# Kernel optimization log

Measured on AMD Instinct MI355X. Metric: run time of the kernel, lower is better.

## Reference

```python
import jax, jax.numpy as jnp
import numpy as np


def setup_inputs() -> dict:
    key = jax.random.key(0)
    k1, k2 = jax.random.split(key)
    B, C, H, W = 4, 64, 256, 256
    x = jax.random.normal(k1, (B, C, H, W), dtype=jnp.float32)
    perspective = jax.random.uniform(k2, (B, 1, H, W), dtype=jnp.float32)
    alpha = jnp.ones((1,), dtype=jnp.float32) * 3.0   # sigma scale
    beta = jnp.ones((1,), dtype=jnp.float32)          # sigmoid slope
    gamma = jnp.zeros((1,), dtype=jnp.float32)        # sigmoid shift
    return {"x": x, "perspective": perspective, "alpha": alpha,
            "beta": beta, "gamma": gamma, "kernel_size": 7}


def reference(x, perspective, alpha, beta, gamma, kernel_size):
    K = int(kernel_size)
    pad = K // 2
    B, C, H, W = x.shape
    # AdaptiveSigmoid sigma map, clamped like the torch module
    sigma = jnp.maximum(alpha * jax.nn.sigmoid(beta * perspective + gamma), 1e-4)  # [B,1,H,W]
    inv2s2 = 1.0 / (2.0 * sigma * sigma)                                           # [B,1,H,W]
    # squared distance of each kernel tap from center (static)
    offs = np.arange(K) - pad
    d2 = (offs[:, None] ** 2 + offs[None, :] ** 2).reshape(-1).astype(np.float32)  # [K*K]
    # per-pixel, per-tap Gaussian weights, normalized over taps
    w = jnp.exp(-d2[:, None, None, None, None] * inv2s2[None])  # [K*K,B,1,H,W]
    w = w / jnp.sum(w, axis=0)
    xp = jnp.pad(x, ((0, 0), (0, 0), (pad, pad), (pad, pad)))
    out = jnp.zeros_like(x)
    k = 0
    for i in range(K):            # fixed small K*K loop (49 taps), jit-friendly
        for j in range(K):
            out = out + w[k] * xp[:, :, i:i + H, j:j + W]
            k += 1
    return out
```

## Files before the change

kernel.cpp:

```cpp
#include <hip/hip_runtime.h>

#define NB 4
#define NC 64
#define NH 256
#define NW 256
#define TH 32
#define SROWS (TH + 6)
#define LROW 264

__global__ __launch_bounds__(256)
void wprep(const float* __restrict__ persp,
           const float* __restrict__ alpha_p,
           const float* __restrict__ beta_p,
           const float* __restrict__ gamma_p,
           float* __restrict__ ws)
{
    const float alpha = alpha_p[0];
    const float beta  = beta_p[0];
    const float gamma = gamma_p[0];
    const int i = (blockIdx.x * 256 + threadIdx.x) * 4;
    const float4 p = *(const float4*)(persp + i);
    const float pa[4] = {p.x, p.y, p.z, p.w};
    float g[4], inv2[4];
    #pragma unroll
    for (int k = 0; k < 4; ++k) {
        const float z  = fmaf(beta, pa[k], gamma);
        const float sg = __builtin_amdgcn_rcpf(1.0f + __expf(-z));
        const float sigma = fmaxf(alpha * sg, 1e-4f);
        const float t  = 0.5f * __builtin_amdgcn_rcpf(sigma * sigma);
        const float gg = __expf(-t);
        const float g2 = gg * gg;
        const float p4 = g2 * g2;
        const float p9 = p4 * p4 * gg;
        const float S  = fmaf(2.0f, (gg + p4) + p9, 1.0f);
        const float inv = __builtin_amdgcn_rcpf(S);
        g[k] = gg;
        inv2[k] = inv * inv;
    }
    float* wp = ws + (size_t)i * 2;
    *(float4*)(wp)     = make_float4(g[0], inv2[0], g[1], inv2[1]);
    *(float4*)(wp + 4) = make_float4(g[2], inv2[2], g[3], inv2[3]);
}

__global__ __launch_bounds__(256, 2)
void adaptive_gauss7(const float* __restrict__ x,
                     const float* __restrict__ wsr,
                     float* __restrict__ out)
{
    __shared__ float lds[SROWS * LROW];

    const int tid  = threadIdx.x;
    const int lane = tid & 63;
    const int wv   = tid >> 6;
    const int c    = blockIdx.x;
    const int h0   = blockIdx.y * TH;
    const int b    = blockIdx.z;
    const int colbase = lane * 4;
    const int rg      = h0 + wv * 8;

    const float* xc   = x   + (size_t)(b * NC + c) * NH * NW;
    float*       outp = out + (size_t)(b * NC + c) * NH * NW;
    const float* wrow = wsr + (size_t)b * NH * NW * 2;

    if (tid < SROWS) {
        *(float4*)&lds[tid * LROW]       = make_float4(0.f, 0.f, 0.f, 0.f);
        *(float4*)&lds[tid * LROW + 260] = make_float4(0.f, 0.f, 0.f, 0.f);
    }

    for (int r = wv; r < SROWS; r += 4) {
        const int gr = h0 - 3 + r;
        if ((unsigned)gr < NH) {
            __builtin_amdgcn_global_load_lds(
                (const __attribute__((address_space(1))) void*)(xc + (size_t)gr * NW + colbase),
                (__attribute__((address_space(3))) void*)&lds[r * LROW + 4],
                16, 0, 0);
        } else {
            *(float4*)&lds[r * LROW + 4 + colbase] = make_float4(0.f, 0.f, 0.f, 0.f);
        }
    }
    __syncthreads();

    float win[7][12];
    #pragma unroll
    for (int r = 0; r < 7; ++r) {
        const float* rp = &lds[(wv * 8 + r) * LROW + colbase];
        const float4 a0 = *(const float4*)(rp);
        const float4 a1 = *(const float4*)(rp + 4);
        const float4 a2 = *(const float4*)(rp + 8);
        win[r][0] = a0.x; win[r][1] = a0.y; win[r][2]  = a0.z; win[r][3]  = a0.w;
        win[r][4] = a1.x; win[r][5] = a1.y; win[r][6]  = a1.z; win[r][7]  = a1.w;
        win[r][8] = a2.x; win[r][9] = a2.y; win[r][10] = a2.z; win[r][11] = a2.w;
    }

    const float* wp0 = wrow + ((size_t)rg * NW + colbase) * 2;
    float4 wa = *(const float4*)(wp0);
    float4 wb = *(const float4*)(wp0 + 4);

    #pragma unroll
    for (int o = 0; o < 8; ++o) {
        float nxt[12];
        if (o < 7) {
            const float* rp = &lds[(wv * 8 + o + 7) * LROW + colbase];
            const float4 a0 = *(const float4*)(rp);
            const float4 a1 = *(const float4*)(rp + 4);
            const float4 a2 = *(const float4*)(rp + 8);
            nxt[0] = a0.x; nxt[1] = a0.y; nxt[2]  = a0.z; nxt[3]  = a0.w;
            nxt[4] = a1.x; nxt[5] = a1.y; nxt[6]  = a1.z; nxt[7]  = a1.w;
            nxt[8] = a2.x; nxt[9] = a2.y; nxt[10] = a2.z; nxt[11] = a2.w;
        }
        float4 na, nb;
        if (o < 7) {
            const float* wp = wrow + ((size_t)(rg + o + 1) * NW + colbase) * 2;
            na = *(const float4*)(wp);
            nb = *(const float4*)(wp + 4);
        }

        const float gk[4] = {wa.x, wa.z, wb.x, wb.z};
        const float iv[4] = {wa.y, wa.w, wb.y, wb.w};
        float res[4];
        #pragma unroll
        for (int k = 0; k < 4; ++k) {
            const float g  = gk[k];
            const float g2 = g * g;
            const float p4 = g2 * g2;
            const float p9 = p4 * p4 * g;

            float rs[7];
            #pragma unroll
            for (int j = 0; j < 7; ++j) {
                const int s = (o + j) % 7;
                rs[j] = fmaf(p9, win[s][k+1] + win[s][k+7],
                        fmaf(p4, win[s][k+2] + win[s][k+6],
                        fmaf(g,  win[s][k+3] + win[s][k+5],
                                 win[s][k+4])));
            }
            const float acc = fmaf(p9, rs[0] + rs[6],
                              fmaf(p4, rs[1] + rs[5],
                              fmaf(g,  rs[2] + rs[4],
                                       rs[3])));
            res[k] = acc * iv[k];
        }
        *(float4*)(outp + (size_t)(rg + o) * NW + colbase) =
            make_float4(res[0], res[1], res[2], res[3]);

        if (o < 7) {
            #pragma unroll
            for (int q = 0; q < 12; ++q)
                win[o % 7][q] = nxt[q];
            wa = na; wb = nb;
        }
    }
}

extern "C" void kernel_launch(void* const* d_in, const int* in_sizes, int n_in,
                              void* d_out, int out_size, void* d_ws, size_t ws_size,
                              hipStream_t stream) {
    const float* x     = (const float*)d_in[0];
    const float* persp = (const float*)d_in[1];
    const float* alpha = (const float*)d_in[2];
    const float* beta  = (const float*)d_in[3];
    const float* gamma = (const float*)d_in[4];
    float* outp        = (float*)d_out;
    float* ws          = (float*)d_ws;

    wprep<<<dim3((NB * NH * NW) / 1024), dim3(256), 0, stream>>>(persp, alpha, beta, gamma, ws);
    adaptive_gauss7<<<dim3(NC, NH / TH, NB), dim3(256), 0, stream>>>(x, ws, outp);
}
```

Measured before the change: 137.6 us.

## Halve row tile and compute output rows in pairs streaming LDS rows once

The row tile shrinks from 32 to 16, so each wave produces 4 output rows instead of 8 and the grid gets twice as many blocks. Instead of keeping a rotating 7-row register window, each pair of output rows streams 8 LDS rows once and accumulates symmetric vertical partial sums on the fly. Weight loads for all four rows are issued before the LDS fill to hide global latency. The aim is lower register pressure and more parallelism, at the cost of a larger halo-overhead fraction (22/16 rows loaded vs 38/32) and more LDS reads per output.

```diff
diff --git a/kernel.cpp b/kernel.cpp
--- a/kernel.cpp
+++ b/kernel.cpp
@@ -4,7 +4,7 @@
 #define NC 64
 #define NH 256
 #define NW 256
-#define TH 32
+#define TH 16
 #define SROWS (TH + 6)
 #define LROW 264
 
@@ -56,11 +56,19 @@
     const int h0   = blockIdx.y * TH;
     const int b    = blockIdx.z;
     const int colbase = lane * 4;
-    const int rg      = h0 + wv * 8;
+    const int rg      = h0 + wv * 4;
 
     const float* xc   = x   + (size_t)(b * NC + c) * NH * NW;
     float*       outp = out + (size_t)(b * NC + c) * NH * NW;
     const float* wrow = wsr + (size_t)b * NH * NW * 2;
+
+    float4 wsv[8];
+    #pragma unroll
+    for (int o = 0; o < 4; ++o) {
+        const float* wp = wrow + ((size_t)(rg + o) * NW + colbase) * 2;
+        wsv[2 * o]     = *(const float4*)(wp);
+        wsv[2 * o + 1] = *(const float4*)(wp + 4);
+    }
 
     if (tid < SROWS) {
         *(float4*)&lds[tid * LROW]       = make_float4(0.f, 0.f, 0.f, 0.f);
@@ -80,75 +88,86 @@
     }
     __syncthreads();
 
-    float win[7][12];
     #pragma unroll
-    for (int r = 0; r < 7; ++r) {
-        const float* rp = &lds[(wv * 8 + r) * LROW + colbase];
-        const float4 a0 = *(const float4*)(rp);
-        const float4 a1 = *(const float4*)(rp + 4);
-        const float4 a2 = *(const float4*)(rp + 8);
-        win[r][0] = a0.x; win[r][1] = a0.y; win[r][2]  = a0.z; win[r][3]  = a0.w;
-        win[r][4] = a1.x; win[r][5] = a1.y; win[r][6]  = a1.z; win[r][7]  = a1.w;
-        win[r][8] = a2.x; win[r][9] = a2.y; win[r][10] = a2.z; win[r][11] = a2.w;
-    }
+    for (int half = 0; half < 2; ++half) {
+        const int o0 = 2 * half;
+        const float4 wa0 = wsv[2 * o0],     wb0 = wsv[2 * o0 + 1];
+        const float4 wa1 = wsv[2 * o0 + 2], wb1 = wsv[2 * o0 + 3];
+        const float g0_[4] = {wa0.x, wa0.z, wb0.x, wb0.z};
+        const float i0_[4] = {wa0.y, wa0.w, wb0.y, wb0.w};
+        const float g1_[4] = {wa1.x, wa1.z, wb1.x, wb1.z};
+        const float i1_[4] = {wa1.y, wa1.w, wb1.y, wb1.w};
+        float g0[4], p40[4], p90[4], g1[4], p41[4], p91[4];
+        #pragma unroll
+        for (int k = 0; k < 4; ++k) {
+            g0[k] = g0_[k];
+            const float t = g0[k] * g0[k];
+            p40[k] = t * t;
+            p90[k] = p40[k] * p40[k] * g0[k];
+            g1[k] = g1_[k];
+            const float u = g1[k] * g1[k];
+            p41[k] = u * u;
+            p91[k] = p41[k] * p41[k] * g1[k];
+        }
 
-    const float* wp0 = wrow + ((size_t)rg * NW + colbase) * 2;
-    float4 wa = *(const float4*)(wp0);
-    float4 wb = *(const float4*)(wp0 + 4);
+        float s0_0[4], s0_1[4], s0_2[4], s0_3[4];
+        float s1_0[4], s1_1[4], s1_2[4], s1_3[4];
 
-    #pragma unroll
-    for (int o = 0; o < 8; ++o) {
-        float nxt[12];
-        if (o < 7) {
-            const float* rp = &lds[(wv * 8 + o + 7) * LROW + colbase];
+        #pragma unroll
+        for (int r = 0; r < 8; ++r) {
+            const float* rp = &lds[(wv * 4 + o0 + r) * LROW + colbase];
             const float4 a0 = *(const float4*)(rp);
             const float4 a1 = *(const float4*)(rp + 4);
             const float4 a2 = *(const float4*)(rp + 8);
-            nxt[0] = a0.x; nxt[1] = a0.y; nxt[2]  = a0.z; nxt[3]  = a0.w;
-            nxt[4] = a1.x; nxt[5] = a1.y; nxt[6]  = a1.z; nxt[7]  = a1.w;
-            nxt[8] = a2.x; nxt[9] = a2.y; nxt[10] = a2.z; nxt[11] = a2.w;
-        }
-        float4 na, nb;
-        if (o < 7) {
-            const float* wp = wrow + ((size_t)(rg + o + 1) * NW + colbase) * 2;
-            na = *(const float4*)(wp);
-            nb = *(const float4*)(wp + 4);
+            const float w[12] = {a0.x, a0.y, a0.z, a0.w,
+                                 a1.x, a1.y, a1.z, a1.w,
+                                 a2.x, a2.y, a2.z, a2.w};
+            #pragma unroll
+            for (int k = 0; k < 4; ++k) {
+                if (r < 7) {
+                    const float rs = fmaf(p90[k], w[k + 1] + w[k + 7],
+                                     fmaf(p40[k], w[k + 2] + w[k + 6],
+                                     fmaf(g0[k],  w[k + 3] + w[k + 5],
+                                                  w[k + 4])));
+                    if      (r == 0) s0_0[k] = rs;
+                    else if (r == 1) s0_1[k] = rs;
+                    else if (r == 2) s0_2[k] = rs;
+                    else if (r == 3) s0_3[k] = rs;
+                    else if (r == 4) s0_2[k] = s0_2[k] + rs;
+                    else if (r == 5) s0_1[k] = s0_1[k] + rs;
+                    else             s0_0[k] = s0_0[k] + rs;
+                }
+                if (r >= 1) {
+                    const float rs = fmaf(p91[k], w[k + 1] + w[k + 7],
+                                     fmaf(p41[k], w[k + 2] + w[k + 6],
+                                     fmaf(g1[k],  w[k + 3] + w[k + 5],
+                                                  w[k + 4])));
+                    const int j = r - 1;
+                    if      (j == 0) s1_0[k] = rs;
+                    else if (j == 1) s1_1[k] = rs;
+                    else if (j == 2) s1_2[k] = rs;
+                    else if (j == 3) s1_3[k] = rs;
+                    else if (j == 4) s1_2[k] = s1_2[k] + rs;
+                    else if (j == 5) s1_1[k] = s1_1[k] + rs;
+                    else             s1_0[k] = s1_0[k] + rs;
+                }
+            }
         }
 
-        const float gk[4] = {wa.x, wa.z, wb.x, wb.z};
-        const float iv[4] = {wa.y, wa.w, wb.y, wb.w};
-        float res[4];
+        float res0[4], res1[4];
         #pragma unroll
         for (int k = 0; k < 4; ++k) {
-            const float g  = gk[k];
-            const float g2 = g * g;
-            const float p4 = g2 * g2;
-            const float p9 = p4 * p4 * g;
-
-            float rs[7];
-            #pragma unroll
-            for (int j = 0; j < 7; ++j) {
-                const int s = (o + j) % 7;
-                rs[j] = fmaf(p9, win[s][k+1] + win[s][k+7],
-                        fmaf(p4, win[s][k+2] + win[s][k+6],
-                        fmaf(g,  win[s][k+3] + win[s][k+5],
-                                 win[s][k+4])));
-            }
-            const float acc = fmaf(p9, rs[0] + rs[6],
-                              fmaf(p4, rs[1] + rs[5],
-                              fmaf(g,  rs[2] + rs[4],
-                                       rs[3])));
-            res[k] = acc * iv[k];
+            res0[k] = fmaf(p90[k], s0_0[k],
+                      fmaf(p40[k], s0_1[k],
+                      fmaf(g0[k],  s0_2[k], s0_3[k]))) * i0_[k];
+            res1[k] = fmaf(p91[k], s1_0[k],
+                      fmaf(p41[k], s1_1[k],
+                      fmaf(g1[k],  s1_2[k], s1_3[k]))) * i1_[k];
         }
-        *(float4*)(outp + (size_t)(rg + o) * NW + colbase) =
-            make_float4(res[0], res[1], res[2], res[3]);
-
-        if (o < 7) {
-            #pragma unroll
-            for (int q = 0; q < 12; ++q)
-                win[o % 7][q] = nxt[q];
-            wa = na; wb = nb;
-        }
+        *(float4*)(outp + (size_t)(rg + o0) * NW + colbase) =
+            make_float4(res0[0], res0[1], res0[2], res0[3]);
+        *(float4*)(outp + (size_t)(rg + o0 + 1) * NW + colbase) =
+            make_float4(res1[0], res1[1], res1[2], res1[3]);
     }
 }
 
```

New measurement: 153.7 us. 11.7% more time.
